# Performance work log

Measured on AMD Instinct MI355X. Metric: run time of the kernel, lower is better.

Reference implementation:

```python
import jax, jax.numpy as jnp
import numpy as np

N, E, G = 50000, 500000, 512
IN_C, HID, EXTRA = 6, 32, 4
EPS = 1e-5


def setup_inputs() -> dict:
    key = jax.random.key(0)
    ks = jax.random.split(key, 24)
    rn = lambda k, s, sc=0.1: jax.random.normal(k, s, jnp.float32) * sc
    return {
        "x": jax.random.normal(ks[0], (N, IN_C), jnp.float32),
        "edge_index": jax.random.randint(ks[1], (2, E), 0, N),
        "edge_attr": jax.random.normal(ks[2], (E, 5), jnp.float32),
        "batch": jnp.sort(jax.random.randint(ks[3], (N,), 0, G)),
        "graph_attr": jax.random.normal(ks[4], (G, EXTRA), jnp.float32),
        # edge MLP 1: 5 -> 32 -> IN_C*HID
        "e1_w1": rn(ks[5], (5, 32)), "e1_b1": jnp.zeros((32,), jnp.float32),
        "e1_w2": rn(ks[6], (32, IN_C * HID)), "e1_b2": jnp.zeros((IN_C * HID,), jnp.float32),
        "root1": rn(ks[7], (IN_C, HID)), "bias1": jnp.zeros((HID,), jnp.float32),
        "bn1_g": jnp.ones((HID,), jnp.float32), "bn1_b": jnp.zeros((HID,), jnp.float32),
        # edge MLP 2: 5 -> 32 -> HID*HID
        "e2_w1": rn(ks[8], (5, 32)), "e2_b1": jnp.zeros((32,), jnp.float32),
        "e2_w2": rn(ks[9], (32, HID * HID)), "e2_b2": jnp.zeros((HID * HID,), jnp.float32),
        "root2": rn(ks[10], (HID, HID)), "bias2": jnp.zeros((HID,), jnp.float32),
        "bn2_g": jnp.ones((HID,), jnp.float32), "bn2_b": jnp.zeros((HID,), jnp.float32),
        "fc_w": rn(ks[11], (HID + EXTRA, 3)), "fc_b": jnp.zeros((3,), jnp.float32),
    }


def _nnconv(x, src, dst, edge_attr, w1, b1, w2, b2, root, bias, in_c, out_c):
    # per-edge weight matrix from edge MLP
    h = jax.nn.relu(edge_attr @ w1 + b1)                    # [E, 32]
    W = (h @ w2 + b2).reshape(-1, in_c, out_c)              # [E, in_c, out_c]
    msg = jnp.einsum('ei,eio->eo', x[src], W)               # per-edge matvec
    agg = jax.ops.segment_sum(msg, dst, num_segments=N)
    cnt = jax.ops.segment_sum(jnp.ones((msg.shape[0],), msg.dtype), dst, num_segments=N)
    agg = agg / jnp.maximum(cnt, 1.0)[:, None]              # scatter-mean
    return agg + x @ root + bias


def _bn(x, g, b):
    mu = jnp.mean(x, axis=0)
    var = jnp.mean(jnp.square(x - mu), axis=0)
    return (x - mu) * jax.lax.rsqrt(var + EPS) * g + b


def reference(x, edge_index, edge_attr, batch, graph_attr,
              e1_w1, e1_b1, e1_w2, e1_b2, root1, bias1, bn1_g, bn1_b,
              e2_w1, e2_b1, e2_w2, e2_b2, root2, bias2, bn2_g, bn2_b,
              fc_w, fc_b):
    src, dst = edge_index[0], edge_index[1]
    h = _nnconv(x, src, dst, edge_attr, e1_w1, e1_b1, e1_w2, e1_b2, root1, bias1, IN_C, HID)
    h = jax.nn.relu(_bn(h, bn1_g, bn1_b))  # dropout = identity (eval)
    h = _nnconv(h, src, dst, edge_attr, e2_w1, e2_b1, e2_w2, e2_b2, root2, bias2, HID, HID)
    h = jax.nn.relu(_bn(h, bn2_g, bn2_b))
    # global mean pool over graphs
    psum = jax.ops.segment_sum(h, batch, num_segments=G)
    pcnt = jax.ops.segment_sum(jnp.ones((N,), h.dtype), batch, num_segments=G)
    pooled = psum / jnp.maximum(pcnt, 1.0)[:, None]
    combined = jnp.concatenate([pooled, graph_attr], axis=1)  # [G, HID+EXTRA]
    return combined @ fc_w + fc_b                              # [G, 3]
```

## Files before the change

### kernel.cpp

```cpp
#include <hip/hip_runtime.h>

#define NN 50000
#define EE 500000
#define GG 512

typedef _Float16 f16x8 __attribute__((ext_vector_type(8)));
typedef _Float16 f16x2 __attribute__((ext_vector_type(2)));
typedef float f32x16 __attribute__((ext_vector_type(16)));

union F16x8U { f16x8 v8; f16x2 v2[4]; unsigned u[4]; };

__device__ __forceinline__ unsigned splat_h(float a){
  return __builtin_bit_cast(unsigned, __builtin_amdgcn_cvt_pkrtz(a, a));
}

__device__ __forceinline__ void gload16(const _Float16* g, _Float16* l){
  __builtin_amdgcn_global_load_lds(
      (const __attribute__((address_space(1))) unsigned int*)g,
      (__attribute__((address_space(3))) unsigned int*)l, 16, 0, 0);
}

#define NL1 (20*512)
#define NL2 (72*512)
__launch_bounds__(256)
__global__ void prep_k(const float* __restrict__ x,
                       const float* __restrict__ w2a, const float* __restrict__ b2a,
                       const float* __restrict__ w2b, const float* __restrict__ b2b,
                       _Float16* __restrict__ xh, _Float16* __restrict__ BtL1,
                       _Float16* __restrict__ BtL2)
{
  int idx = blockIdx.x*256 + threadIdx.x;
  if (idx < NL1){
    int t = idx >> 9, r = idx & 511;
    int lane = r >> 3, j = r & 7;
    int col = lane & 31, hi = lane >> 5;
    int ki = 16*t + 8*hi + j;
    int k = ki >> 3, i = ki & 7;
    float v = 0.f;
    if (i < 6){
      if (k < 32)       v = w2a[k*192 + i*32 + col];
      else if (k == 32) v = b2a[i*32 + col];
    }
    BtL1[idx] = (_Float16)v;
  } else if (idx < NL1 + NL2){
    int q = idx - NL1;
    int t = q >> 9, r = q & 511;
    int lane = r >> 3, j = r & 7;
    int col = lane & 31, hi = lane >> 5;
    int ki = 16*t + 8*hi + j;
    int k = ki >> 5, i = ki & 31;
    float v = 0.f;
    if (k < 32)       v = w2b[k*1024 + i*32 + col];
    else if (k == 32) v = b2b[i*32 + col];
    BtL2[q] = (_Float16)v;
  } else {
    int j = idx - (NL1 + NL2);
    if (j < NN*8){
      int n = j >> 3, i = j & 7;
      xh[j] = (_Float16)((i < 6) ? x[n*6 + i] : 0.f);
    }
  }
}

__launch_bounds__(256)
__global__ void hist_k(const int* __restrict__ ei, int* __restrict__ hist)
{
  int e = blockIdx.x*256 + threadIdx.x;
  if (e < EE) atomicAdd(&hist[ei[EE + e]], 1);
}

__launch_bounds__(256)
__global__ void scan1_k(const int* __restrict__ hist, int* __restrict__ part,
                        int* __restrict__ blk)
{
  __shared__ int s[256];
  int t = threadIdx.x, b = blockIdx.x, i = b*256 + t;
  int v = (i < NN) ? hist[i] : 0;
  s[t] = v; __syncthreads();
  #pragma unroll
  for (int off = 1; off < 256; off <<= 1){
    int u = (t >= off) ? s[t-off] : 0;
    __syncthreads();
    s[t] += u;
    __syncthreads();
  }
  if (i < NN) part[i] = s[t] - v;
  if (t == 255) blk[b] = s[255];
}

__launch_bounds__(256)
__global__ void scan2_k(int* __restrict__ blk, int nblk)
{
  __shared__ int s[256];
  int t = threadIdx.x;
  int v = (t < nblk) ? blk[t] : 0;
  s[t] = v; __syncthreads();
  #pragma unroll
  for (int off = 1; off < 256; off <<= 1){
    int u = (t >= off) ? s[t-off] : 0;
    __syncthreads();
    s[t] += u;
    __syncthreads();
  }
  if (t < nblk) blk[t] = s[t] - v;
}

__launch_bounds__(256)
__global__ void rowptr_k(const int* __restrict__ part, const int* __restrict__ blk,
                         int* __restrict__ rowptr)
{
  int n = blockIdx.x*256 + threadIdx.x;
  if (n < NN) rowptr[n] = part[n] + blk[n >> 8];
}

__launch_bounds__(256)
__global__ void scatter_k(const int* __restrict__ ei, const float* __restrict__ ea,
                          const int* __restrict__ rowptr, int* __restrict__ cursor,
                          int* __restrict__ esrc, int* __restrict__ edst,
                          float* __restrict__ eap)
{
  int e = blockIdx.x*256 + threadIdx.x;
  if (e < EE){
    int d = ei[EE + e];
    int slot = rowptr[d] + atomicAdd(&cursor[d], 1);
    esrc[slot] = ei[e];
    edst[slot] = d;
    #pragma unroll
    for (int q = 0; q < 5; ++q) eap[(long)slot*5 + q] = ea[(long)e*5 + q];
  }
}

template<int CONV>
__launch_bounds__(256, 4)
__global__ void conv_msg_k(const _Float16* __restrict__ xh,
                           const int* __restrict__ esrc,
                           const int* __restrict__ edst,
                           const float* __restrict__ eap,
                           const float* __restrict__ w1,
                           const float* __restrict__ b1,
                           const _Float16* __restrict__ Btg,
                           const int* __restrict__ rowptr,
                           const int* __restrict__ deg,
                           float* __restrict__ agg)
{
  constexpr int BTB_F16 = (CONV == 1) ? 10240 : 8192;
  __shared__ unsigned hs2[128][37];
  __shared__ _Float16 btb[BTB_F16];
  __shared__ int segrow[130];
  __shared__ int segcnt[2];

  const int tid  = threadIdx.x;
  const int lane = tid & 63;
  const int wave = tid >> 6;
  const int e0   = blockIdx.x * 128;
  const int nvalid = (EE - e0 < 128) ? (EE - e0) : 128;

  if (CONV == 1){
    #pragma unroll
    for (int i = 0; i < 5; ++i)
      gload16(Btg + (wave + 4*i)*512 + lane*8, btb + (wave + 4*i)*512);
  } else {
    gload16(Btg + wave*512 + lane*8,       btb + wave*512);
    gload16(Btg + (wave + 4)*512 + lane*8, btb + (wave + 4)*512);
  }

  {
    int e  = tid >> 1;
    int kb = (tid & 1) * 16;
    int eg = e0 + e;
    bool valid = eg < EE;
    float eav[5];
    #pragma unroll
    for (int q = 0; q < 5; ++q) eav[q] = valid ? eap[(long)eg*5 + q] : 0.f;
    #pragma unroll
    for (int k = kb; k < kb + 16; ++k){
      float a = b1[k];
      #pragma unroll
      for (int q = 0; q < 5; ++q) a += eav[q] * w1[q*32 + k];
      hs2[e][k] = splat_h(fmaxf(a, 0.f));
    }
    if (kb == 16){
      hs2[e][32] = splat_h(1.f);
      hs2[e][33] = 0u; hs2[e][34] = 0u; hs2[e][35] = 0u;
    }
  }
  __syncthreads();

  const int col = lane & 31;
  const int hi  = lane >> 5;
  const int el  = wave*32 + col;
  const int emy = e0 + el;
  const int src = (emy < EE) ? esrc[emy] : 0;

  F16x8U xa, xb;
  if (CONV == 1){
    xa.v8 = *(const f16x8*)(xh + (long)src*8);
    xb.v8 = xa.v8;
  } else {
    xa.v8 = *(const f16x8*)(xh + (long)src*32 + 8*hi);
    xb.v8 = *(const f16x8*)(xh + (long)src*32 + 16 + 8*hi);
  }

  unsigned h2[(CONV == 1) ? 18 : 34];
  if (CONV == 1){
    #pragma unroll
    for (int t = 0; t < 18; ++t) h2[t] = hs2[el][2*t + hi];
  } else {
    #pragma unroll
    for (int kk = 0; kk < 34; ++kk) h2[kk] = hs2[el][kk];
  }

  f32x16 acc;
  #pragma unroll
  for (int r = 0; r < 16; ++r) acc[r] = 0.f;

  if (CONV == 1){
    #pragma unroll
    for (int t = 0; t < 18; ++t){
      f16x8 bf = *(const f16x8*)&btb[t*512 + lane*8];
      f16x2 hv = __builtin_bit_cast(f16x2, h2[t]);
      F16x8U af;
      #pragma unroll
      for (int p = 0; p < 4; ++p) af.v2[p] = hv * xa.v2[p];
      acc = __builtin_amdgcn_mfma_f32_32x32x16_f16(af.v8, bf, acc, 0, 0, 0);
    }
    __syncthreads();
  } else {
    #pragma unroll
    for (int c = 0; c < 9; ++c){
      if (c < 8){
        const _Float16* gs = Btg + (long)((c+1)*8 + wave)*512 + lane*8;
        _Float16* ls = btb + ((c+1)&1)*4096 + wave*512;
        gload16(gs, ls);
        gload16(gs + 4*512, ls + 4*512);
      }
      const int tmax = (c == 8) ? 4 : 8;
      #pragma unroll
      for (int tt = 0; tt < tmax; ++tt){
        const int t = c*8 + tt;
        f16x8 bf = *(const f16x8*)&btb[(c&1)*4096 + tt*512 + lane*8];
        f16x2 hv = __builtin_bit_cast(f16x2, h2[t >> 1]);
        const F16x8U& xs = (t & 1) ? xb : xa;
        F16x8U af;
        #pragma unroll
        for (int p = 0; p < 4; ++p) af.v2[p] = hv * xs.v2[p];
        acc = __builtin_amdgcn_mfma_f32_32x32x16_f16(af.v8, bf, acc, 0, 0, 0);
      }
      __syncthreads();
    }
  }

  float* msg = (float*)&hs2[0][0];

  #pragma unroll
  for (int g = 0; g < 4; ++g){
    #pragma unroll
    for (int r = 0; r < 4; ++r){
      int row = wave*32 + r + 8*g + 4*hi;
      msg[row*37 + col] = acc[4*g + r];
    }
  }

  bool st = false;
  if (tid < 128){
    int eg = e0 + tid;
    st = (tid < nvalid) && (tid == 0 || edst[eg] != edst[eg-1]);
  }
  unsigned long long m = __ballot(st);
  int rank = __popcll(m & ((1ull << lane) - 1ull));
  if (tid < 128 && lane == 0) segcnt[wave] = (int)__popcll(m);
  __syncthreads();
  if (st) segrow[rank + ((tid >= 64) ? segcnt[0] : 0)] = tid;
  if (tid == 128) segrow[segcnt[0] + segcnt[1]] = nvalid;
  __syncthreads();

  const int nseg = segcnt[0] + segcnt[1];
  const int c2 = tid & 31;
  for (int s = tid >> 5; s < nseg; s += 8){
    int r0 = segrow[s], r1 = segrow[s+1];
    float sum = 0.f;
    for (int r = r0; r < r1; ++r) sum += msg[r*37 + c2];
    int d  = edst[e0 + r0];
    int rp = rowptr[d];
    if (rp >= e0 && rp + deg[d] <= e0 + nvalid)
      agg[(long)d*32 + c2] = sum;
    else
      atomicAdd(&agg[(long)d*32 + c2], sum);
  }
}

template<int IN_C>
__launch_bounds__(256)
__global__ void node_update_k(const float* __restrict__ xin, const float* __restrict__ root,
                              const float* __restrict__ bias, const int* __restrict__ cnt,
                              float* __restrict__ buf, float* __restrict__ stats, int N)
{
  __shared__ float rs[IN_C*32];
  __shared__ float bs[32];
  __shared__ float redS[4][32], redQ[4][32];
  int tid = threadIdx.x;
  for (int i = tid; i < IN_C*32; i += 256) rs[i] = root[i];
  if (tid < 32) bs[tid] = bias[tid];
  __syncthreads();
  int o = tid & 31, slot = tid >> 5;
  float s = 0.f, q = 0.f;
  for (int n = blockIdx.x*8 + slot; n < N; n += gridDim.x*8){
    float c = fmaxf((float)cnt[n], 1.f);
    float v = buf[(long)n*32 + o] / c + bs[o];
    const float* xrow = &xin[(long)n*IN_C];
    #pragma unroll
    for (int i = 0; i < IN_C; ++i) v += xrow[i] * rs[i*32 + o];
    buf[(long)n*32 + o] = v;
    s += v; q += v*v;
  }
  s += __shfl_xor(s, 32); q += __shfl_xor(q, 32);
  int wv = tid >> 6;
  if ((tid & 63) < 32){ redS[wv][o] = s; redQ[wv][o] = q; }
  __syncthreads();
  if (tid < 32){
    float ts = 0.f, tq = 0.f;
    #pragma unroll
    for (int w = 0; w < 4; ++w){ ts += redS[w][tid]; tq += redQ[w][tid]; }
    atomicAdd(&stats[tid], ts); atomicAdd(&stats[32 + tid], tq);
  }
}

__launch_bounds__(256)
__global__ void bn_relu_k(float* __restrict__ buf, _Float16* __restrict__ bufh,
                          const float* __restrict__ stats,
                          const float* __restrict__ gg, const float* __restrict__ bb,
                          float invN, int total)
{
  int i = blockIdx.x*256 + threadIdx.x;
  if (i < total){
    int o = i & 31;
    float mu  = stats[o] * invN;
    float var = stats[32+o] * invN - mu*mu;
    float v = fmaxf((buf[i] - mu) * rsqrtf(var + 1e-5f) * gg[o] + bb[o], 0.f);
    buf[i]  = v;
    bufh[i] = (_Float16)v;
  }
}

__launch_bounds__(256)
__global__ void bn_pool_k(const float* __restrict__ buf, const float* __restrict__ stats,
                          const float* __restrict__ gg, const float* __restrict__ bb,
                          const int* __restrict__ batch, float* __restrict__ psum,
                          float* __restrict__ pcnt, float invN, int N)
{
  constexpr int NPB  = 512;
  constexpr int MAXG = 33;
  __shared__ float gsum[MAXG][33];
  int tid = threadIdx.x;
  int n0  = blockIdx.x * NPB;
  for (int i = tid; i < MAXG*33; i += 256) (&gsum[0][0])[i] = 0.f;
  __syncthreads();

  int o = tid & 31, slot = tid >> 5;
  int gfirst = batch[n0];
  float mu  = stats[o] * invN;
  float var = stats[32+o] * invN - mu*mu;
  float sc  = rsqrtf(var + 1e-5f) * gg[o];
  float sh  = bb[o] - mu*sc;
  int nend  = (N - n0 < NPB) ? N : n0 + NPB;

  float acc = 0.f, cacc = 0.f;
  int curls = -1;
  for (int n = n0 + slot; n < nend; n += 8){
    int ls = batch[n] - gfirst;
    float v = fmaxf(buf[(long)n*32 + o]*sc + sh, 0.f);
    if (ls != curls){
      if (curls >= 0){
        if ((unsigned)curls < MAXG){
          if (acc  != 0.f) atomicAdd(&gsum[curls][o], acc);
          if (o == 0 && cacc != 0.f) atomicAdd(&gsum[curls][32], cacc);
        } else {
          if (acc  != 0.f) atomicAdd(&psum[(long)(gfirst+curls)*32 + o], acc);
          if (o == 0 && cacc != 0.f) atomicAdd(&pcnt[gfirst+curls], cacc);
        }
      }
      acc = 0.f; cacc = 0.f; curls = ls;
    }
    acc += v;
    if (o == 0) cacc += 1.f;
  }
  if (curls >= 0){
    if ((unsigned)curls < MAXG){
      if (acc  != 0.f) atomicAdd(&gsum[curls][o], acc);
      if (o == 0 && cacc != 0.f) atomicAdd(&gsum[curls][32], cacc);
    } else {
      if (acc  != 0.f) atomicAdd(&psum[(long)(gfirst+curls)*32 + o], acc);
      if (o == 0 && cacc != 0.f) atomicAdd(&pcnt[gfirst+curls], cacc);
    }
  }
  __syncthreads();

  for (int i = tid; i < MAXG*32; i += 256){
    int ls = i >> 5, c = i & 31;
    float v = gsum[ls][c];
    if (v != 0.f) atomicAdd(&psum[(long)(gfirst+ls)*32 + c], v);
  }
  if (tid < MAXG){
    float v = gsum[tid][32];
    if (v != 0.f) atomicAdd(&pcnt[gfirst + tid], v);
  }
}

__launch_bounds__(256)
__global__ void final_k(const float* __restrict__ psum, const float* __restrict__ pcnt,
                        const float* __restrict__ gattr, const float* __restrict__ fcw,
                        const float* __restrict__ fcb, float* __restrict__ out, int G)
{
  int g = blockIdx.x*256 + threadIdx.x;
  if (g < G){
    float c = fmaxf(pcnt[g], 1.f);
    float o0 = fcb[0], o1 = fcb[1], o2 = fcb[2];
    #pragma unroll
    for (int j = 0; j < 32; ++j){
      float p = psum[g*32+j] / c;
      o0 += p*fcw[j*3+0]; o1 += p*fcw[j*3+1]; o2 += p*fcw[j*3+2];
    }
    #pragma unroll
    for (int j = 0; j < 4; ++j){
      float a = gattr[g*4+j];
      o0 += a*fcw[(32+j)*3+0]; o1 += a*fcw[(32+j)*3+1]; o2 += a*fcw[(32+j)*3+2];
    }
    out[g*3+0] = o0; out[g*3+1] = o1; out[g*3+2] = o2;
  }
}

extern "C" void kernel_launch(void* const* d_in, const int* in_sizes, int n_in,
                              void* d_out, int out_size, void* d_ws, size_t ws_size,
                              hipStream_t stream)
{
  const float* x     = (const float*)d_in[0];
  const int*   ei    = (const int*)  d_in[1];
  const float* ea    = (const float*)d_in[2];
  const int*   batch = (const int*)  d_in[3];
  const float* gattr = (const float*)d_in[4];
  const float* e1_w1 = (const float*)d_in[5];
  const float* e1_b1 = (const float*)d_in[6];
  const float* e1_w2 = (const float*)d_in[7];
  const float* e1_b2 = (const float*)d_in[8];
  const float* root1 = (const float*)d_in[9];
  const float* bias1 = (const float*)d_in[10];
  const float* bn1_g = (const float*)d_in[11];
  const float* bn1_b = (const float*)d_in[12];
  const float* e2_w1 = (const float*)d_in[13];
  const float* e2_b1 = (const float*)d_in[14];
  const float* e2_w2 = (const float*)d_in[15];
  const float* e2_b2 = (const float*)d_in[16];
  const float* root2 = (const float*)d_in[17];
  const float* bias2 = (const float*)d_in[18];
  const float* bn2_g = (const float*)d_in[19];
  const float* bn2_b = (const float*)d_in[20];
  const float* fc_w  = (const float*)d_in[21];
  const float* fc_b  = (const float*)d_in[22];
  float* out = (float*)d_out;

  float* ws = (float*)d_ws;
  const long NM = (long)NN*32;
  const int NBLK = (NN + 255) / 256;

  float* bufA   = ws;
  float* bufB   = bufA + NM;
  float* stats  = bufB + NM;
  float* psum   = stats + 128;
  float* pcnt   = psum + GG*32;
  int*   hist   = (int*)(pcnt + GG);
  int*   cursor = hist + NN;
  long zero_elems = 2*NM + 128 + GG*32 + GG + 2L*NN;
  int*   part   = cursor + NN;
  int*   blk    = part + NN;
  int*   rowptr = blk + 256;
  int*   esrc   = rowptr + NN;
  int*   edst   = esrc + EE;
  float* eap    = (float*)(edst + EE);
  _Float16* bufAh = (_Float16*)(eap + (long)EE*5);
  _Float16* xh    = bufAh + NM;
  _Float16* BtL1  = xh + (long)NN*8;
  _Float16* BtL2  = BtL1 + NL1;

  (void)hipMemsetAsync(d_ws, 0, (size_t)zero_elems * 4, stream);

  const int PREP_ELEMS = NL1 + NL2 + NN*8;
  prep_k<<<(PREP_ELEMS + 255)/256, 256, 0, stream>>>(x, e1_w2, e1_b2, e2_w2, e2_b2,
                                                     xh, BtL1, BtL2);

  const int EGRID = (EE + 255)/256;
  hist_k<<<EGRID, 256, 0, stream>>>(ei, hist);
  scan1_k<<<NBLK, 256, 0, stream>>>(hist, part, blk);
  scan2_k<<<1, 256, 0, stream>>>(blk, NBLK);
  rowptr_k<<<NBLK, 256, 0, stream>>>(part, blk, rowptr);
  scatter_k<<<EGRID, 256, 0, stream>>>(ei, ea, rowptr, cursor, esrc, edst, eap);

  const int EBLK = (EE + 127) / 128;
  conv_msg_k<1><<<EBLK, 256, 0, stream>>>(xh, esrc, edst, eap, e1_w1, e1_b1, BtL1,
                                          rowptr, hist, bufA);
  node_update_k<6><<<256, 256, 0, stream>>>(x, root1, bias1, hist, bufA, stats, NN);
  bn_relu_k<<<(int)((NM + 255)/256), 256, 0, stream>>>(bufA, bufAh, stats, bn1_g, bn1_b,
                                                       1.f/NN, (int)NM);
  conv_msg_k<2><<<EBLK, 256, 0, stream>>>(bufAh, esrc, edst, eap, e2_w1, e2_b1, BtL2,
                                          rowptr, hist, bufB);
  node_update_k<32><<<256, 256, 0, stream>>>(bufA, root2, bias2, hist, bufB, stats + 64, NN);
  bn_pool_k<<<(NN + 511)/512, 256, 0, stream>>>(bufB, stats + 64, bn2_g, bn2_b, batch,
                                                psum, pcnt, 1.f/NN, NN);
  final_k<<<2, 256, 0, stream>>>(psum, pcnt, gattr, fc_w, fc_b, out, GG);
}
```

Before: 319.7 us.

## Process 256 edges per 512-thread conv block, trim padded MFMA steps, vectorize root matvec

The message kernel now runs 512 threads per block and covers 256 edges per block. Each wave loads fewer shared B-tiles per stage, which halves the number of blocks and the per-block staging of the basis matrices. The K loop drops one MFMA step per convolution, which looks like it skips padding slices. The node update kernel reads root inputs as float2/float4 and launches twice as many blocks. Risks are doubled LDS per block, which limits how many blocks fit per CU, and the tighter register budget implied by launch_bounds(512,4), which could cause spills.

```diff
diff --git a/kernel.cpp b/kernel.cpp
--- a/kernel.cpp
+++ b/kernel.cpp
@@ -131,7 +131,7 @@
 }
 
 template<int CONV>
-__launch_bounds__(256, 4)
+__launch_bounds__(512, 4)
 __global__ void conv_msg_k(const _Float16* __restrict__ xh,
                            const int* __restrict__ esrc,
                            const int* __restrict__ edst,
@@ -144,24 +144,25 @@
                            float* __restrict__ agg)
 {
   constexpr int BTB_F16 = (CONV == 1) ? 10240 : 8192;
-  __shared__ unsigned hs2[128][37];
+  __shared__ unsigned hs2[256][37];
   __shared__ _Float16 btb[BTB_F16];
-  __shared__ int segrow[130];
-  __shared__ int segcnt[2];
+  __shared__ int segrow[258];
+  __shared__ int segcnt[4];
 
   const int tid  = threadIdx.x;
   const int lane = tid & 63;
   const int wave = tid >> 6;
-  const int e0   = blockIdx.x * 128;
-  const int nvalid = (EE - e0 < 128) ? (EE - e0) : 128;
+  const int e0   = blockIdx.x * 256;
+  const int nvalid = (EE - e0 < 256) ? (EE - e0) : 256;
 
   if (CONV == 1){
     #pragma unroll
-    for (int i = 0; i < 5; ++i)
-      gload16(Btg + (wave + 4*i)*512 + lane*8, btb + (wave + 4*i)*512);
+    for (int i = 0; i < 3; ++i){
+      int s = wave + 8*i;
+      if (s < 20) gload16(Btg + (long)s*512 + lane*8, btb + s*512);
+    }
   } else {
-    gload16(Btg + wave*512 + lane*8,       btb + wave*512);
-    gload16(Btg + (wave + 4)*512 + lane*8, btb + (wave + 4)*512);
+    gload16(Btg + (long)wave*512 + lane*8, btb + wave*512);
   }
 
   {
@@ -201,13 +202,13 @@
     xb.v8 = *(const f16x8*)(xh + (long)src*32 + 16 + 8*hi);
   }
 
-  unsigned h2[(CONV == 1) ? 18 : 34];
+  unsigned h2[(CONV == 1) ? 17 : 33];
   if (CONV == 1){
     #pragma unroll
-    for (int t = 0; t < 18; ++t) h2[t] = hs2[el][2*t + hi];
+    for (int t = 0; t < 17; ++t) h2[t] = hs2[el][2*t + hi];
   } else {
     #pragma unroll
-    for (int kk = 0; kk < 34; ++kk) h2[kk] = hs2[el][kk];
+    for (int kk = 0; kk < 33; ++kk) h2[kk] = hs2[el][kk];
   }
 
   f32x16 acc;
@@ -216,7 +217,7 @@
 
   if (CONV == 1){
     #pragma unroll
-    for (int t = 0; t < 18; ++t){
+    for (int t = 0; t < 17; ++t){
       f16x8 bf = *(const f16x8*)&btb[t*512 + lane*8];
       f16x2 hv = __builtin_bit_cast(f16x2, h2[t]);
       F16x8U af;
@@ -229,12 +230,10 @@
     #pragma unroll
     for (int c = 0; c < 9; ++c){
       if (c < 8){
-        const _Float16* gs = Btg + (long)((c+1)*8 + wave)*512 + lane*8;
-        _Float16* ls = btb + ((c+1)&1)*4096 + wave*512;
-        gload16(gs, ls);
-        gload16(gs + 4*512, ls + 4*512);
+        gload16(Btg + (long)((c+1)*8 + wave)*512 + lane*8,
+                btb + ((c+1)&1)*4096 + wave*512);
       }
-      const int tmax = (c == 8) ? 4 : 8;
+      const int tmax = (c == 8) ? 2 : 8;
       #pragma unroll
       for (int tt = 0; tt < tmax; ++tt){
         const int t = c*8 + tt;
@@ -262,21 +261,26 @@
   }
 
   bool st = false;
-  if (tid < 128){
+  if (tid < 256){
     int eg = e0 + tid;
     st = (tid < nvalid) && (tid == 0 || edst[eg] != edst[eg-1]);
   }
   unsigned long long m = __ballot(st);
   int rank = __popcll(m & ((1ull << lane) - 1ull));
-  if (tid < 128 && lane == 0) segcnt[wave] = (int)__popcll(m);
-  __syncthreads();
-  if (st) segrow[rank + ((tid >= 64) ? segcnt[0] : 0)] = tid;
-  if (tid == 128) segrow[segcnt[0] + segcnt[1]] = nvalid;
-  __syncthreads();
-
-  const int nseg = segcnt[0] + segcnt[1];
+  if (tid < 256 && lane == 0) segcnt[wave] = (int)__popcll(m);
+  __syncthreads();
+  int nseg = segcnt[0] + segcnt[1] + segcnt[2] + segcnt[3];
+  if (st){
+    int off = 0;
+    #pragma unroll
+    for (int w = 0; w < 3; ++w) if (w < wave) off += segcnt[w];
+    segrow[rank + off] = tid;
+  }
+  if (tid == 256) segrow[nseg] = nvalid;
+  __syncthreads();
+
   const int c2 = tid & 31;
-  for (int s = tid >> 5; s < nseg; s += 8){
+  for (int s = tid >> 5; s < nseg; s += 16){
     int r0 = segrow[s], r1 = segrow[s+1];
     float sum = 0.f;
     for (int r = r0; r < r1; ++r) sum += msg[r*37 + c2];
@@ -307,9 +311,22 @@
   for (int n = blockIdx.x*8 + slot; n < N; n += gridDim.x*8){
     float c = fmaxf((float)cnt[n], 1.f);
     float v = buf[(long)n*32 + o] / c + bs[o];
-    const float* xrow = &xin[(long)n*IN_C];
-    #pragma unroll
-    for (int i = 0; i < IN_C; ++i) v += xrow[i] * rs[i*32 + o];
+    if constexpr (IN_C == 32){
+      const float4* xr = (const float4*)&xin[(long)n*32];
+      #pragma unroll
+      for (int i4 = 0; i4 < 8; ++i4){
+        float4 xv = xr[i4];
+        v += xv.x*rs[(i4*4+0)*32+o] + xv.y*rs[(i4*4+1)*32+o]
+           + xv.z*rs[(i4*4+2)*32+o] + xv.w*rs[(i4*4+3)*32+o];
+      }
+    } else {
+      const float2* xr = (const float2*)&xin[(long)n*6];
+      #pragma unroll
+      for (int i2 = 0; i2 < 3; ++i2){
+        float2 xv = xr[i2];
+        v += xv.x*rs[(i2*2+0)*32+o] + xv.y*rs[(i2*2+1)*32+o];
+      }
+    }
     buf[(long)n*32 + o] = v;
     s += v; q += v*v;
   }
@@ -494,15 +511,15 @@
   rowptr_k<<<NBLK, 256, 0, stream>>>(part, blk, rowptr);
   scatter_k<<<EGRID, 256, 0, stream>>>(ei, ea, rowptr, cursor, esrc, edst, eap);
 
-  const int EBLK = (EE + 127) / 128;
-  conv_msg_k<1><<<EBLK, 256, 0, stream>>>(xh, esrc, edst, eap, e1_w1, e1_b1, BtL1,
+  const int EBLK = (EE + 255) / 256;
+  conv_msg_k<1><<<EBLK, 512, 0, stream>>>(xh, esrc, edst, eap, e1_w1, e1_b1, BtL1,
                                           rowptr, hist, bufA);
-  node_update_k<6><<<256, 256, 0, stream>>>(x, root1, bias1, hist, bufA, stats, NN);
+  node_update_k<6><<<512, 256, 0, stream>>>(x, root1, bias1, hist, bufA, stats, NN);
   bn_relu_k<<<(int)((NM + 255)/256), 256, 0, stream>>>(bufA, bufAh, stats, bn1_g, bn1_b,
                                                        1.f/NN, (int)NM);
-  conv_msg_k<2><<<EBLK, 256, 0, stream>>>(bufAh, esrc, edst, eap, e2_w1, e2_b1, BtL2,
+  conv_msg_k<2><<<EBLK, 512, 0, stream>>>(bufAh, esrc, edst, eap, e2_w1, e2_b1, BtL2,
                                           rowptr, hist, bufB);
-  node_update_k<32><<<256, 256, 0, stream>>>(bufA, root2, bias2, hist, bufB, stats + 64, NN);
+  node_update_k<32><<<512, 256, 0, stream>>>(bufA, root2, bias2, hist, bufB, stats + 64, NN);
   bn_pool_k<<<(NN + 511)/512, 256, 0, stream>>>(bufB, stats + 64, bn2_g, bn2_b, batch,
                                                 psum, pcnt, 1.f/NN, NN);
   final_k<<<2, 256, 0, stream>>>(psum, pcnt, gattr, fc_w, fc_b, out, GG);
```

Result: no change. 321.0 us (+0.4%).
